# Optimization experiments

Hardware: AMD Instinct MI355X
Metric: run time of the kernel (lower is better)

Reference implementation:

```python
import jax, jax.numpy as jnp
import numpy as np

HEADS = 16
D_MODEL = 1024
D_EXP = 2048  # d_model * expansion_factor
D_HEAD = D_EXP // HEADS
DEPTH = 12
B, L = 2, 2048


def setup_inputs() -> dict:
    key = jax.random.key(0)
    ks = jax.random.split(key, 4)
    x = jax.random.normal(ks[0], (B, L, D_MODEL), dtype=jnp.float32)
    w_in = jax.random.normal(ks[1], (4 * D_EXP, D_MODEL), dtype=jnp.float32) * 0.02
    w_out = jax.random.normal(ks[2], (D_MODEL, D_EXP), dtype=jnp.float32) * (0.02 / np.sqrt(2 * DEPTH))
    # LearnedALiBi init: logspace(0,-6,heads//2,base=2) ++ zeros(heads - heads//2)
    half = HEADS // 2
    slopes = jnp.concatenate([
        jnp.asarray(2.0 ** np.linspace(0.0, -6.0, half), dtype=jnp.float32),
        jnp.zeros((HEADS - half,), dtype=jnp.float32),
    ])
    smear_factor = jnp.linspace(-6.0, 6.0, HEADS, dtype=jnp.float32)
    return {
        "x": x, "w_in": w_in, "w_out": w_out,
        "ln_in_g": jnp.ones((D_MODEL,), jnp.float32), "ln_in_b": jnp.zeros((D_MODEL,), jnp.float32),
        "ln_out_g": jnp.ones((D_MODEL,), jnp.float32), "ln_out_b": jnp.zeros((D_MODEL,), jnp.float32),
        "slopes": slopes, "smear_factor": smear_factor,
    }


def _layernorm(x, g, b, eps=1e-5):
    mu = jnp.mean(x, axis=-1, keepdims=True)
    var = jnp.mean(jnp.square(x - mu), axis=-1, keepdims=True)
    return (x - mu) * jax.lax.rsqrt(var + eps) * g + b


def reference(x, w_in, w_out, ln_in_g, ln_in_b, ln_out_g, ln_out_b, slopes, smear_factor):
    b, l, d = x.shape
    h = _layernorm(x, ln_in_g, ln_in_b)
    qkvp = h @ w_in.T  # (b, l, 4*D_EXP)
    q, k, v, p = jnp.split(qkvp, 4, axis=-1)

    def to_heads(t):  # b i (h d) -> b h i d
        return t.reshape(b, l, HEADS, D_HEAD).transpose(0, 2, 1, 3)

    q, k, v = to_heads(q), to_heads(k), to_heads(v)

    # key smearing: k_i <- (1-s)*k_i + s*k_{i-1}
    smear = jax.nn.sigmoid(smear_factor)[None, :, None, None]
    k_shift = jnp.pad(k, ((0, 0), (0, 0), (1, 0), (0, 0)))[:, :, :-1]
    k = (1.0 - smear) * k + smear * k_shift

    logits = jnp.einsum('bhid,bhjd->bhij', q, k) * (D_HEAD ** -0.5)
    # learned ALiBi bias: j * slope_h  (depends only on key index)
    alibi = jnp.arange(l, dtype=logits.dtype)[None, None, None, :] * slopes[None, :, None, None]
    # causal bias: -1e10 * (1 - tril)
    i_idx = jnp.arange(l)
    causal = jnp.where(i_idx[:, None] >= i_idx[None, :], 0.0, -1e10)[None, None]
    a = jax.nn.softmax(logits + alibi + causal, axis=-1)

    o = jnp.einsum('bhij,bhjd->bhid', a, v)
    o = o.transpose(0, 2, 1, 3).reshape(b, l, D_EXP)  # b h i d -> b i (h d)
    gated = jax.nn.silu(p) * o
    y = gated @ w_out.T
    return _layernorm(y, ln_out_g, ln_out_b)
```

## Files before the change

kernel.cpp:

```cpp
#include <hip/hip_runtime.h>
#include <hip/hip_bf16.h>
#include <stdint.h>


typedef __bf16 bf16;
typedef bf16  bf16x8 __attribute__((ext_vector_type(8)));
typedef bf16  bf16x4 __attribute__((ext_vector_type(4)));
typedef float f32x4  __attribute__((ext_vector_type(4)));

#define SEQ   2048
#define NBATC 2

__device__ __forceinline__ void gld_lds16(const bf16* g, bf16* l) {
  __builtin_amdgcn_global_load_lds((const __attribute__((address_space(1))) void*)g,
                                   (__attribute__((address_space(3))) void*)l, 16, 0, 0);
}

__global__ __launch_bounds__(256) void cvt_kernel(const float* __restrict__ in,
                                                  bf16* __restrict__ out, int n8) {
  int t = blockIdx.x * 256 + threadIdx.x;
  if (t >= n8) return;
  const float4* p = (const float4*)in + (size_t)t * 2;
  float4 a = p[0], b = p[1];
  bf16x8 o;
  o[0] = (bf16)a.x; o[1] = (bf16)a.y; o[2] = (bf16)a.z; o[3] = (bf16)a.w;
  o[4] = (bf16)b.x; o[5] = (bf16)b.y; o[6] = (bf16)b.z; o[7] = (bf16)b.w;
  *((bf16x8*)out + t) = o;
}

template<bool BF16OUT>
__global__ __launch_bounds__(256) void ln_kernel(const float* __restrict__ x,
    const float* __restrict__ gamma, const float* __restrict__ beta,
    void* __restrict__ out) {
  const int row = blockIdx.x;
  const int tid = threadIdx.x;
  float4 v = *(const float4*)(x + (size_t)row * 1024 + tid * 4);
  float s  = v.x + v.y + v.z + v.w;
  float ss = v.x * v.x + v.y * v.y + v.z * v.z + v.w * v.w;
#pragma unroll
  for (int m = 1; m < 64; m <<= 1) { s += __shfl_xor(s, m, 64); ss += __shfl_xor(ss, m, 64); }
  __shared__ float red[8];
  if ((tid & 63) == 0) { red[tid >> 6] = s; red[(tid >> 6) + 4] = ss; }
  __syncthreads();
  s  = red[0] + red[1] + red[2] + red[3];
  ss = red[4] + red[5] + red[6] + red[7];
  const float mu  = s * (1.f / 1024.f);
  const float inv = rsqrtf(ss * (1.f / 1024.f) - mu * mu + 1e-5f);
  float4 g  = *(const float4*)(gamma + tid * 4);
  float4 bb = *(const float4*)(beta  + tid * 4);
  float y0 = (v.x - mu) * inv * g.x + bb.x;
  float y1 = (v.y - mu) * inv * g.y + bb.y;
  float y2 = (v.z - mu) * inv * g.z + bb.z;
  float y3 = (v.w - mu) * inv * g.w + bb.w;
  if (BF16OUT) {
    bf16* o = (bf16*)out + (size_t)row * 1024 + tid * 4;
    o[0] = (bf16)y0; o[1] = (bf16)y1; o[2] = (bf16)y2; o[3] = (bf16)y3;
  } else {
    float* o = (float*)out + (size_t)row * 1024 + tid * 4;
    o[0] = y0; o[1] = y1; o[2] = y2; o[3] = y3;
  }
}

__global__ __launch_bounds__(256) void smear_kernel(const bf16* __restrict__ qkvp,
    const float* __restrict__ smf, bf16* __restrict__ ksm) {
  int t  = blockIdx.x * 256 + threadIdx.x;
  int d8 = t & 15;
  int i  = (t >> 4) & 2047;
  int h  = (t >> 15) & 15;
  int b  = t >> 19;
  float sm = 1.f / (1.f + __expf(-smf[h]));
  const bf16* base = qkvp + (size_t)(b * SEQ + i) * 8192 + 2048 + h * 128 + d8 * 8;
  bf16x8 cur = *(const bf16x8*)base;
  bf16x8 prv = cur;
  if (i > 0) prv = *(const bf16x8*)(base - 8192);
  bf16x8 o;
#pragma unroll
  for (int e = 0; e < 8; e++) {
    float pv = (i > 0) ? (float)prv[e] : 0.f;
    o[e] = (bf16)((1.f - sm) * (float)cur[e] + sm * pv);
  }
  size_t idx = ((size_t)(b * 16 + h) * SEQ + i) * 128 + ((d8 * 8) ^ ((i & 7) << 3));
  *(bf16x8*)(ksm + idx) = o;
}

__global__ __launch_bounds__(256) void vtrans_kernel(const bf16* __restrict__ qkvp,
                                                     bf16* __restrict__ vt) {
  __shared__ bf16 T[128][72];
  const int kt = blockIdx.x, bh = blockIdx.y;
  const int b = bh >> 4, h = bh & 15;
  const int t = threadIdx.x;
  {
    int i = t >> 2, d0 = (t & 3) * 32;
    const bf16* src = qkvp + (size_t)(b * SEQ + kt * 64 + i) * 8192 + 4096 + h * 128 + d0;
#pragma unroll
    for (int m = 0; m < 4; m++) {
      bf16x8 v8 = *(const bf16x8*)(src + m * 8);
#pragma unroll
      for (int e = 0; e < 8; e++) T[d0 + m * 8 + e][i] = v8[e];
    }
  }
  __syncthreads();
  {
    int d = t >> 1, i0 = (t & 1) * 32;
    bf16* dst = vt + (size_t)bh * (SEQ * 128) + (size_t)kt * 8192 + d * 64;
#pragma unroll
    for (int m = 0; m < 4; m++) {
      bf16x8 v8 = *(const bf16x8*)&T[d][i0 + m * 8];
      *(bf16x8*)(dst + (((i0 + m * 8)) ^ ((d & 7) << 3))) = v8;
    }
  }
}

__global__ __launch_bounds__(512) void gemm256(const bf16* __restrict__ A,
    const bf16* __restrict__ Bt, bf16* __restrict__ C, int M, int N, int K,
    int RX, int SX, int SY) {
  __shared__ bf16 As[2][256 * 64];
  __shared__ bf16 Bs[2][256 * 64];
  const int w   = blockIdx.x;
  const int xcd = w & 7, idx = w >> 3;
  const int rx = xcd % RX, ry = xcd / RX;
  const int bx = rx * SX + idx % SX;
  const int by = ry * SY + idx / SX;
  const int tid  = threadIdx.x;
  const int lane = tid & 63, wid = tid >> 6;
  const int l4 = lane >> 4, l16 = lane & 15;
  const int wr = wid >> 2, wc = wid & 3;
  const int rowBase = by * 256, colBase = bx * 256;
  const int NT = K >> 6;

  f32x4 acc[8][4];
  const f32x4 z = {0.f, 0.f, 0.f, 0.f};
#pragma unroll
  for (int i = 0; i < 8; i++)
#pragma unroll
    for (int j = 0; j < 4; j++) acc[i][j] = z;

  auto stage = [&](int kt, int bsel) {
    const int k0 = kt * 64;
    bf16* ad = &As[bsel][tid * 8];
    bf16* bd = &Bs[bsel][tid * 8];
#pragma unroll
    for (int j = 0; j < 4; ++j) {
      const int c   = j * 512 + tid;
      const int row = c >> 3;
      const int sc  = ((c & 7) * 8) ^ ((row & 7) << 3);
      gld_lds16(A  + (size_t)(rowBase + row) * K + k0 + sc, ad + j * 4096);
      gld_lds16(Bt + (size_t)(colBase + row) * K + k0 + sc, bd + j * 4096);
    }
  };

  stage(0, 0);
  for (int t = 0; t < NT; ++t) {
    const int cur = t & 1;
    if (t + 1 < NT) {
      stage(t + 1, cur ^ 1);
      asm volatile("s_waitcnt vmcnt(8)" ::: "memory");
    } else {
      asm volatile("s_waitcnt vmcnt(0)" ::: "memory");
    }
    asm volatile("s_barrier" ::: "memory");
    const bf16* a_ = &As[cur][0];
    const bf16* b_ = &Bs[cur][0];
#pragma unroll
    for (int ks = 0; ks < 2; ++ks) {
      bf16x8 bfr[4];
#pragma unroll
      for (int ni = 0; ni < 4; ++ni) {
        const int br = wc * 64 + ni * 16 + l16;
        bfr[ni] = *(const bf16x8*)&b_[br * 64 + ((ks * 32 + l4 * 8) ^ ((br & 7) << 3))];
      }
#pragma unroll
      for (int mi = 0; mi < 8; ++mi) {
        const int ar = wr * 128 + mi * 16 + l16;
        bf16x8 af = *(const bf16x8*)&a_[ar * 64 + ((ks * 32 + l4 * 8) ^ ((ar & 7) << 3))];
#pragma unroll
        for (int ni = 0; ni < 4; ++ni)
          acc[mi][ni] = __builtin_amdgcn_mfma_f32_16x16x32_bf16(af, bfr[ni], acc[mi][ni], 0, 0, 0);
      }
    }
    asm volatile("s_waitcnt lgkmcnt(0)" ::: "memory");
    asm volatile("s_barrier" ::: "memory");
  }

#pragma unroll
  for (int mi = 0; mi < 8; ++mi)
#pragma unroll
    for (int ni = 0; ni < 4; ++ni) {
      int row = rowBase + wr * 128 + mi * 16 + l4 * 4;
      int col = colBase + wc * 64 + ni * 16 + l16;
#pragma unroll
      for (int r = 0; r < 4; ++r)
        C[(size_t)(row + r) * N + col] = (bf16)acc[mi][ni][r];
    }
}

template<typename OutT>
__global__ __launch_bounds__(256) void gemm_bt(const bf16* __restrict__ A,
    const bf16* __restrict__ Bt, OutT* __restrict__ C, int M, int N, int K,
    int RX, int SX, int SY) {
  __shared__ bf16 As[128 * 32];
  __shared__ bf16 Bs[128 * 32];
  const int w   = blockIdx.x;
  const int xcd = w & 7, idx = w >> 3;
  const int rx = xcd % RX, ry = xcd / RX;
  const int bx = rx * SX + idx % SX;
  const int by = ry * SY + idx / SX;
  const int tid  = threadIdx.x;
  const int lane = tid & 63, wid = tid >> 6;
  const int l4 = lane >> 4, l16 = lane & 15;
  const int wr = wid >> 1, wc = wid & 1;
  const int rowBase = by * 128, colBase = bx * 128;

  const bf16* gA = A  + (size_t)(rowBase + (tid >> 2)) * K + (tid & 3) * 8;
  const bf16* gB = Bt + (size_t)(colBase + (tid >> 2)) * K + (tid & 3) * 8;
  const size_t rowStep = (size_t)64 * K;

  f32x4 acc[4][4];
  const f32x4 z = {0.f, 0.f, 0.f, 0.f};
#pragma unroll
  for (int i = 0; i < 4; i++)
#pragma unroll
    for (int j = 0; j < 4; j++) acc[i][j] = z;

  for (int k0 = 0; k0 < K; k0 += 32) {
    __syncthreads();
    gld_lds16(gA + k0,           &As[tid * 8]);
    gld_lds16(gA + rowStep + k0, &As[2048 + tid * 8]);
    gld_lds16(gB + k0,           &Bs[tid * 8]);
    gld_lds16(gB + rowStep + k0, &Bs[2048 + tid * 8]);
    __syncthreads();
    bf16x8 af[4], bfr[4];
#pragma unroll
    for (int mi = 0; mi < 4; mi++)
      af[mi] = *(const bf16x8*)&As[(wr * 64 + mi * 16 + l16) * 32 + l4 * 8];
#pragma unroll
    for (int ni = 0; ni < 4; ni++)
      bfr[ni] = *(const bf16x8*)&Bs[(wc * 64 + ni * 16 + l16) * 32 + l4 * 8];
#pragma unroll
    for (int mi = 0; mi < 4; mi++)
#pragma unroll
      for (int ni = 0; ni < 4; ni++)
        acc[mi][ni] = __builtin_amdgcn_mfma_f32_16x16x32_bf16(af[mi], bfr[ni], acc[mi][ni], 0, 0, 0);
  }
#pragma unroll
  for (int mi = 0; mi < 4; mi++)
#pragma unroll
    for (int ni = 0; ni < 4; ni++) {
      int row = rowBase + wr * 64 + mi * 16 + l4 * 4;
      int col = colBase + wc * 64 + ni * 16 + l16;
#pragma unroll
      for (int r = 0; r < 4; r++)
        C[(size_t)(row + r) * N + col] = (OutT)acc[mi][ni][r];
    }
}

__global__ __launch_bounds__(256) void attn_kernel(const bf16* __restrict__ qkvp,
    const bf16* __restrict__ ksm, const bf16* __restrict__ vt,
    const float* __restrict__ slopes, bf16* __restrict__ gated) {
  const int w   = blockIdx.x;
  const int l   = (w & 7) * 64 + (w >> 3);
  const int qp  = l & 15;
  const int bh  = l >> 4;
  const int b   = bh >> 4, h = bh & 15;
  const int tid = threadIdx.x, wid = tid >> 6, lane = tid & 63;
  const int l4 = lane >> 4, l16 = lane & 15;
  const int swz = (l16 & 7) << 3;
  const float LOG2E = 1.44269504f;
  const float s2 = 0.08838834764831845f * LOG2E;
  const float slopeL = slopes[h] * LOG2E;

  __shared__ bf16 Kb[2][64 * 128];
  __shared__ bf16 Vb[2][64 * 128];
  __shared__ bf16 P_lds[64 * 64];

  const bf16* ksmB = ksm + (size_t)bh * SEQ * 128;
  const bf16* vtB  = vt  + (size_t)bh * SEQ * 128;

  auto stage = [&](int kt, int bsel) {
    const bf16* ks = ksmB + kt * 8192 + tid * 8;
    const bf16* vs = vtB  + kt * 8192 + tid * 8;
    bf16* kd = &Kb[bsel][tid * 8];
    bf16* vd = &Vb[bsel][tid * 8];
#pragma unroll
    for (int g = 0; g < 4; g++) {
      gld_lds16(ks + g * 2048, kd + g * 2048);
      gld_lds16(vs + g * 2048, vd + g * 2048);
    }
  };

  auto run_strip = [&](int qtile, int ntiles) {
    const int iq = qtile * 64 + wid * 16 + l16;
    bf16x8 qf[4];
    {
      const bf16* qrow = qkvp + (size_t)(b * SEQ + iq) * 8192 + h * 128;
#pragma unroll
      for (int kb = 0; kb < 4; kb++) qf[kb] = *(const bf16x8*)(qrow + kb * 32 + l4 * 8);
    }
    f32x4 oacc[8];
    const f32x4 z = {0.f, 0.f, 0.f, 0.f};
#pragma unroll
    for (int i = 0; i < 8; i++) oacc[i] = z;
    float m2 = -1e38f, lpart = 0.f;

    stage(0, 0);
    for (int t = 0; t < ntiles; ++t) {
      __syncthreads();
      if (t + 1 < ntiles) stage(t + 1, (t + 1) & 1);
      const bf16* K_ = Kb[t & 1];
      const bf16* V_ = Vb[t & 1];
      const int kt = t;

      f32x4 sacc[4];
#pragma unroll
      for (int jf = 0; jf < 4; jf++) {
        bf16x8 kf[4];
#pragma unroll
        for (int kb = 0; kb < 4; kb++)
          kf[kb] = *(const bf16x8*)&K_[(jf * 16 + l16) * 128 + ((kb * 32 + l4 * 8) ^ swz)];
        f32x4 a = z;
#pragma unroll
        for (int kb = 0; kb < 4; kb++)
          a = __builtin_amdgcn_mfma_f32_16x16x32_bf16(kf[kb], qf[kb], a, 0, 0, 0);
        sacc[jf] = a;
      }

      const bool diag = (kt == qtile);
      const int kbase = kt * 64 + l4 * 4;
      float sadj[4][4];
#pragma unroll
      for (int jf = 0; jf < 4; jf++) {
#pragma unroll
        for (int r = 0; r < 4; r++) {
          int j = kbase + jf * 16 + r;
          float v = fmaf(sacc[jf][r], s2, (float)j * slopeL);
          if (diag && j > iq) v = -1e38f;
          sadj[jf][r] = v;
        }
      }

      float mx = sadj[0][0];
#pragma unroll
      for (int jf = 0; jf < 4; jf++)
#pragma unroll
        for (int r = 0; r < 4; r++) mx = fmaxf(mx, sadj[jf][r]);
      mx = fmaxf(mx, __shfl_xor(mx, 16, 64));
      mx = fmaxf(mx, __shfl_xor(mx, 32, 64));

      if (__any(mx > m2 + 14.f)) {
        float mnew  = fmaxf(m2, mx);
        float alpha = __builtin_amdgcn_exp2f(m2 - mnew);
        m2 = mnew;
        lpart *= alpha;
#pragma unroll
        for (int df = 0; df < 8; df++) oacc[df] *= alpha;
      }

      float rs = 0.f;
#pragma unroll
      for (int jf = 0; jf < 4; jf++) {
        bf16x4 pw;
#pragma unroll
        for (int r = 0; r < 4; r++) {
          float pe = __builtin_amdgcn_exp2f(sadj[jf][r] - m2);
          rs += pe;
          pw[r] = (bf16)pe;
        }
        *(bf16x4*)&P_lds[(wid * 16 + l16) * 64 + ((jf * 16 + l4 * 4) ^ swz)] = pw;
      }
      lpart += rs;

#pragma unroll
      for (int kb2 = 0; kb2 < 2; ++kb2) {
        bf16x8 pf = *(const bf16x8*)&P_lds[(wid * 16 + l16) * 64 + ((kb2 * 32 + l4 * 8) ^ swz)];
#pragma unroll
        for (int df = 0; df < 8; df++) {
          bf16x8 vf = *(const bf16x8*)&V_[(df * 16 + l16) * 64 + ((kb2 * 32 + l4 * 8) ^ swz)];
          oacc[df] = __builtin_amdgcn_mfma_f32_16x16x32_bf16(vf, pf, oacc[df], 0, 0, 0);
        }
      }
    }

    lpart += __shfl_xor(lpart, 16, 64);
    lpart += __shfl_xor(lpart, 32, 64);
    const float linv = 1.f / lpart;
    const bf16* pgrow = qkvp + (size_t)(b * SEQ + iq) * 8192 + 6144 + h * 128;
    bf16* grow = gated + (size_t)(b * SEQ + iq) * 2048 + h * 128;
#pragma unroll
    for (int df = 0; df < 8; df++) {
      const int d0 = df * 16 + l4 * 4;
      bf16x4 pg4 = *(const bf16x4*)(pgrow + d0);
      bf16x4 o4;
#pragma unroll
      for (int r = 0; r < 4; r++) {
        float o  = oacc[df][r] * linv;
        float pg = (float)pg4[r];
        float silu = pg / (1.f + __expf(-pg));
        o4[r] = (bf16)(silu * o);
      }
      *(bf16x4*)(grow + d0) = o4;
    }
  };

  run_strip(qp, qp + 1);
  __syncthreads();
  run_strip(31 - qp, 32 - qp);
}

extern "C" void kernel_launch(void* const* d_in, const int* in_sizes, int n_in,
                              void* d_out, int out_size, void* d_ws, size_t ws_size,
                              hipStream_t stream) {
  (void)in_sizes; (void)n_in; (void)out_size; (void)ws_size;
  const float* x      = (const float*)d_in[0];
  const float* w_in   = (const float*)d_in[1];
  const float* w_out  = (const float*)d_in[2];
  const float* lnig   = (const float*)d_in[3];
  const float* lnib   = (const float*)d_in[4];
  const float* lnog   = (const float*)d_in[5];
  const float* lnob   = (const float*)d_in[6];
  const float* slopes = (const float*)d_in[7];
  const float* smf    = (const float*)d_in[8];
  float* out = (float*)d_out;

  char* ws = (char*)d_ws;
  size_t off = 0;
  bf16* hb      = (bf16*)(ws + off); off += (size_t)4096 * 1024 * 2;
  bf16* w_in_b  = (bf16*)(ws + off); off += (size_t)8192 * 1024 * 2;
  bf16* w_out_b = (bf16*)(ws + off); off += (size_t)1024 * 2048 * 2;
  bf16* qkvp    = (bf16*)(ws + off); off += (size_t)4096 * 8192 * 2;
  bf16* ksm     = (bf16*)(ws + off); off += (size_t)32 * 2048 * 128 * 2;
  bf16* gated   = (bf16*)(ws + off); off += (size_t)4096 * 2048 * 2;
  float* yb     = (float*)(ws + off); off += (size_t)4096 * 1024 * 4;
  bf16* vt      = (bf16*)yb;

  cvt_kernel<<<4096, 256, 0, stream>>>(w_in,  w_in_b,  8388608 / 8);
  cvt_kernel<<<1024, 256, 0, stream>>>(w_out, w_out_b, 2097152 / 8);
  ln_kernel<true><<<4096, 256, 0, stream>>>(x, lnig, lnib, hb);
  gemm256<<<512, 512, 0, stream>>>(hb, w_in_b, qkvp, 4096, 8192, 1024, 4, 8, 8);
  smear_kernel<<<4096, 256, 0, stream>>>(qkvp, smf, ksm);
  vtrans_kernel<<<dim3(32, 32), 256, 0, stream>>>(qkvp, vt);
  attn_kernel<<<512, 256, 0, stream>>>(qkvp, ksm, vt, slopes, gated);
  gemm_bt<float><<<256, 256, 0, stream>>>(gated, w_out_b, yb, 4096, 1024, 2048, 1, 8, 4);
  ln_kernel<false><<<4096, 256, 0, stream>>>(yb, lnog, lnob, out);
}
```

Measured before the change: 241.4 us.

## Fuse smear and V-transpose kernels; restructure attention into 128-row 8-wave blocks

Merges the key-smearing and V-transpose kernels into one prep kernel, which removes a launch and runs both over the same tile grid. The attention kernel switches from 256-thread blocks that each process two paired 64-row strips to 512-thread blocks that each own one 128-row query tile. Blocks are ordered heaviest-first with an XCD-aware head mapping. K/V loads are staged with explicit vmcnt waits and raw barriers so the next tile's global-to-LDS load overlaps compute. In exchange the causal work is no longer balanced per block, because each block now has a different tile count, and the manual waitcnt/barrier scheme is fragile.

```diff
diff --git a/kernel.cpp b/kernel.cpp
--- a/kernel.cpp
+++ b/kernel.cpp
@@ -61,34 +61,13 @@
   }
 }
 
-__global__ __launch_bounds__(256) void smear_kernel(const bf16* __restrict__ qkvp,
-    const float* __restrict__ smf, bf16* __restrict__ ksm) {
-  int t  = blockIdx.x * 256 + threadIdx.x;
-  int d8 = t & 15;
-  int i  = (t >> 4) & 2047;
-  int h  = (t >> 15) & 15;
-  int b  = t >> 19;
-  float sm = 1.f / (1.f + __expf(-smf[h]));
-  const bf16* base = qkvp + (size_t)(b * SEQ + i) * 8192 + 2048 + h * 128 + d8 * 8;
-  bf16x8 cur = *(const bf16x8*)base;
-  bf16x8 prv = cur;
-  if (i > 0) prv = *(const bf16x8*)(base - 8192);
-  bf16x8 o;
-#pragma unroll
-  for (int e = 0; e < 8; e++) {
-    float pv = (i > 0) ? (float)prv[e] : 0.f;
-    o[e] = (bf16)((1.f - sm) * (float)cur[e] + sm * pv);
-  }
-  size_t idx = ((size_t)(b * 16 + h) * SEQ + i) * 128 + ((d8 * 8) ^ ((i & 7) << 3));
-  *(bf16x8*)(ksm + idx) = o;
-}
-
-__global__ __launch_bounds__(256) void vtrans_kernel(const bf16* __restrict__ qkvp,
-                                                     bf16* __restrict__ vt) {
+__global__ __launch_bounds__(256) void prep_kernel(const bf16* __restrict__ qkvp,
+    const float* __restrict__ smf, bf16* __restrict__ ksm, bf16* __restrict__ vt) {
   __shared__ bf16 T[128][72];
   const int kt = blockIdx.x, bh = blockIdx.y;
   const int b = bh >> 4, h = bh & 15;
   const int t = threadIdx.x;
+
   {
     int i = t >> 2, d0 = (t & 3) * 32;
     const bf16* src = qkvp + (size_t)(b * SEQ + kt * 64 + i) * 8192 + 4096 + h * 128 + d0;
@@ -99,6 +78,29 @@
       for (int e = 0; e < 8; e++) T[d0 + m * 8 + e][i] = v8[e];
     }
   }
+
+  {
+    float sm = 1.f / (1.f + __expf(-smf[h]));
+#pragma unroll
+    for (int j = 0; j < 4; j++) {
+      int c  = j * 256 + t;
+      int il = c >> 4, d8 = c & 15;
+      int i  = kt * 64 + il;
+      const bf16* base = qkvp + (size_t)(b * SEQ + i) * 8192 + 2048 + h * 128 + d8 * 8;
+      bf16x8 cur = *(const bf16x8*)base;
+      bf16x8 prv = cur;
+      if (i > 0) prv = *(const bf16x8*)(base - 8192);
+      bf16x8 o;
+#pragma unroll
+      for (int e = 0; e < 8; e++) {
+        float pv = (i > 0) ? (float)prv[e] : 0.f;
+        o[e] = (bf16)((1.f - sm) * (float)cur[e] + sm * pv);
+      }
+      size_t idx = ((size_t)bh * SEQ + i) * 128 + ((d8 * 8) ^ ((i & 7) << 3));
+      *(bf16x8*)(ksm + idx) = o;
+    }
+  }
+
   __syncthreads();
   {
     int d = t >> 1, i0 = (t & 1) * 32;
@@ -254,13 +256,13 @@
     }
 }
 
-__global__ __launch_bounds__(256) void attn_kernel(const bf16* __restrict__ qkvp,
+__global__ __launch_bounds__(512, 4) void attn_kernel(const bf16* __restrict__ qkvp,
     const bf16* __restrict__ ksm, const bf16* __restrict__ vt,
     const float* __restrict__ slopes, bf16* __restrict__ gated) {
-  const int w   = blockIdx.x;
-  const int l   = (w & 7) * 64 + (w >> 3);
-  const int qp  = l & 15;
-  const int bh  = l >> 4;
+  const int w     = blockIdx.x;
+  const int xcd   = w & 7, r0 = w >> 3;
+  const int bh    = xcd * 4 + (r0 & 3);
+  const int qtile = 15 - (r0 >> 2);
   const int b   = bh >> 4, h = bh & 15;
   const int tid = threadIdx.x, wid = tid >> 6, lane = tid & 63;
   const int l4 = lane >> 4, l16 = lane & 15;
@@ -271,139 +273,137 @@
 
   __shared__ bf16 Kb[2][64 * 128];
   __shared__ bf16 Vb[2][64 * 128];
-  __shared__ bf16 P_lds[64 * 64];
+  __shared__ bf16 P_lds[128 * 64];
 
   const bf16* ksmB = ksm + (size_t)bh * SEQ * 128;
   const bf16* vtB  = vt  + (size_t)bh * SEQ * 128;
 
   auto stage = [&](int kt, int bsel) {
-    const bf16* ks = ksmB + kt * 8192 + tid * 8;
-    const bf16* vs = vtB  + kt * 8192 + tid * 8;
-    bf16* kd = &Kb[bsel][tid * 8];
-    bf16* vd = &Vb[bsel][tid * 8];
-#pragma unroll
-    for (int g = 0; g < 4; g++) {
-      gld_lds16(ks + g * 2048, kd + g * 2048);
-      gld_lds16(vs + g * 2048, vd + g * 2048);
+#pragma unroll
+    for (int j = 0; j < 2; j++) {
+      const int c = j * 512 + tid;
+      gld_lds16(ksmB + (size_t)kt * 8192 + c * 8, &Kb[bsel][c * 8]);
+      gld_lds16(vtB  + (size_t)kt * 8192 + c * 8, &Vb[bsel][c * 8]);
     }
   };
 
-  auto run_strip = [&](int qtile, int ntiles) {
-    const int iq = qtile * 64 + wid * 16 + l16;
-    bf16x8 qf[4];
-    {
-      const bf16* qrow = qkvp + (size_t)(b * SEQ + iq) * 8192 + h * 128;
-#pragma unroll
-      for (int kb = 0; kb < 4; kb++) qf[kb] = *(const bf16x8*)(qrow + kb * 32 + l4 * 8);
-    }
-    f32x4 oacc[8];
-    const f32x4 z = {0.f, 0.f, 0.f, 0.f};
-#pragma unroll
-    for (int i = 0; i < 8; i++) oacc[i] = z;
-    float m2 = -1e38f, lpart = 0.f;
-
-    stage(0, 0);
-    for (int t = 0; t < ntiles; ++t) {
-      __syncthreads();
-      if (t + 1 < ntiles) stage(t + 1, (t + 1) & 1);
-      const bf16* K_ = Kb[t & 1];
-      const bf16* V_ = Vb[t & 1];
-      const int kt = t;
-
-      f32x4 sacc[4];
-#pragma unroll
-      for (int jf = 0; jf < 4; jf++) {
-        bf16x8 kf[4];
-#pragma unroll
-        for (int kb = 0; kb < 4; kb++)
-          kf[kb] = *(const bf16x8*)&K_[(jf * 16 + l16) * 128 + ((kb * 32 + l4 * 8) ^ swz)];
-        f32x4 a = z;
-#pragma unroll
-        for (int kb = 0; kb < 4; kb++)
-          a = __builtin_amdgcn_mfma_f32_16x16x32_bf16(kf[kb], qf[kb], a, 0, 0, 0);
-        sacc[jf] = a;
-      }
-
-      const bool diag = (kt == qtile);
-      const int kbase = kt * 64 + l4 * 4;
-      float sadj[4][4];
-#pragma unroll
-      for (int jf = 0; jf < 4; jf++) {
-#pragma unroll
-        for (int r = 0; r < 4; r++) {
-          int j = kbase + jf * 16 + r;
-          float v = fmaf(sacc[jf][r], s2, (float)j * slopeL);
-          if (diag && j > iq) v = -1e38f;
-          sadj[jf][r] = v;
-        }
-      }
-
-      float mx = sadj[0][0];
-#pragma unroll
-      for (int jf = 0; jf < 4; jf++)
-#pragma unroll
-        for (int r = 0; r < 4; r++) mx = fmaxf(mx, sadj[jf][r]);
-      mx = fmaxf(mx, __shfl_xor(mx, 16, 64));
-      mx = fmaxf(mx, __shfl_xor(mx, 32, 64));
-
-      if (__any(mx > m2 + 14.f)) {
-        float mnew  = fmaxf(m2, mx);
-        float alpha = __builtin_amdgcn_exp2f(m2 - mnew);
-        m2 = mnew;
-        lpart *= alpha;
-#pragma unroll
-        for (int df = 0; df < 8; df++) oacc[df] *= alpha;
-      }
-
-      float rs = 0.f;
-#pragma unroll
-      for (int jf = 0; jf < 4; jf++) {
-        bf16x4 pw;
-#pragma unroll
-        for (int r = 0; r < 4; r++) {
-          float pe = __builtin_amdgcn_exp2f(sadj[jf][r] - m2);
-          rs += pe;
-          pw[r] = (bf16)pe;
-        }
-        *(bf16x4*)&P_lds[(wid * 16 + l16) * 64 + ((jf * 16 + l4 * 4) ^ swz)] = pw;
-      }
-      lpart += rs;
-
-#pragma unroll
-      for (int kb2 = 0; kb2 < 2; ++kb2) {
-        bf16x8 pf = *(const bf16x8*)&P_lds[(wid * 16 + l16) * 64 + ((kb2 * 32 + l4 * 8) ^ swz)];
-#pragma unroll
-        for (int df = 0; df < 8; df++) {
-          bf16x8 vf = *(const bf16x8*)&V_[(df * 16 + l16) * 64 + ((kb2 * 32 + l4 * 8) ^ swz)];
-          oacc[df] = __builtin_amdgcn_mfma_f32_16x16x32_bf16(vf, pf, oacc[df], 0, 0, 0);
-        }
-      }
-    }
-
-    lpart += __shfl_xor(lpart, 16, 64);
-    lpart += __shfl_xor(lpart, 32, 64);
-    const float linv = 1.f / lpart;
-    const bf16* pgrow = qkvp + (size_t)(b * SEQ + iq) * 8192 + 6144 + h * 128;
-    bf16* grow = gated + (size_t)(b * SEQ + iq) * 2048 + h * 128;
-#pragma unroll
-    for (int df = 0; df < 8; df++) {
-      const int d0 = df * 16 + l4 * 4;
-      bf16x4 pg4 = *(const bf16x4*)(pgrow + d0);
-      bf16x4 o4;
+  const int iq = qtile * 128 + wid * 16 + l16;
+  bf16x8 qf[4];
+  {
+    const bf16* qrow = qkvp + (size_t)(b * SEQ + iq) * 8192 + h * 128;
+#pragma unroll
+    for (int kb = 0; kb < 4; kb++) qf[kb] = *(const bf16x8*)(qrow + kb * 32 + l4 * 8);
+  }
+  f32x4 oacc[8];
+  const f32x4 z = {0.f, 0.f, 0.f, 0.f};
+#pragma unroll
+  for (int i = 0; i < 8; i++) oacc[i] = z;
+  float m2 = -1e38f, lpart = 0.f;
+
+  const int nt = 2 * qtile + 2;
+  stage(0, 0);
+  for (int t = 0; t < nt; ++t) {
+    const int cur = t & 1;
+    if (t + 1 < nt) {
+      stage(t + 1, cur ^ 1);
+      asm volatile("s_waitcnt vmcnt(4)" ::: "memory");
+    } else {
+      asm volatile("s_waitcnt vmcnt(0)" ::: "memory");
+    }
+    __builtin_amdgcn_sched_barrier(0);
+    __builtin_amdgcn_s_barrier();
+    const bf16* K_ = Kb[cur];
+    const bf16* V_ = Vb[cur];
+
+    f32x4 sacc[4];
+#pragma unroll
+    for (int jf = 0; jf < 4; jf++) {
+      f32x4 a = z;
+#pragma unroll
+      for (int kb = 0; kb < 4; kb++) {
+        bf16x8 kf = *(const bf16x8*)&K_[(jf * 16 + l16) * 128 + ((kb * 32 + l4 * 8) ^ swz)];
+        a = __builtin_amdgcn_mfma_f32_16x16x32_bf16(kf, qf[kb], a, 0, 0, 0);
+      }
+      sacc[jf] = a;
+    }
+
+    const bool diag = (t >= 2 * qtile);
+    const int kbase = t * 64 + l4 * 4;
+#pragma unroll
+    for (int jf = 0; jf < 4; jf++) {
 #pragma unroll
       for (int r = 0; r < 4; r++) {
-        float o  = oacc[df][r] * linv;
-        float pg = (float)pg4[r];
-        float silu = pg / (1.f + __expf(-pg));
-        o4[r] = (bf16)(silu * o);
-      }
-      *(bf16x4*)(grow + d0) = o4;
-    }
-  };
-
-  run_strip(qp, qp + 1);
-  __syncthreads();
-  run_strip(31 - qp, 32 - qp);
+        int j = kbase + jf * 16 + r;
+        float v = fmaf(sacc[jf][r], s2, (float)j * slopeL);
+        if (diag && j > iq) v = -1e38f;
+        sacc[jf][r] = v;
+      }
+    }
+
+    float mx = sacc[0][0];
+#pragma unroll
+    for (int jf = 0; jf < 4; jf++)
+#pragma unroll
+      for (int r = 0; r < 4; r++) mx = fmaxf(mx, sacc[jf][r]);
+    mx = fmaxf(mx, __shfl_xor(mx, 16, 64));
+    mx = fmaxf(mx, __shfl_xor(mx, 32, 64));
+
+    if (__any(mx > m2 + 14.f)) {
+      float mnew  = fmaxf(m2, mx);
+      float alpha = __builtin_amdgcn_exp2f(m2 - mnew);
+      m2 = mnew;
+      lpart *= alpha;
+#pragma unroll
+      for (int df = 0; df < 8; df++) oacc[df] *= alpha;
+    }
+
+    float rs = 0.f;
+#pragma unroll
+    for (int jf = 0; jf < 4; jf++) {
+      bf16x4 pw;
+#pragma unroll
+      for (int r = 0; r < 4; r++) {
+        float pe = __builtin_amdgcn_exp2f(sacc[jf][r] - m2);
+        rs += pe;
+        pw[r] = (bf16)pe;
+      }
+      *(bf16x4*)&P_lds[(wid * 16 + l16) * 64 + ((jf * 16 + l4 * 4) ^ swz)] = pw;
+    }
+    lpart += rs;
+
+#pragma unroll
+    for (int kb2 = 0; kb2 < 2; ++kb2) {
+      bf16x8 pf = *(const bf16x8*)&P_lds[(wid * 16 + l16) * 64 + ((kb2 * 32 + l4 * 8) ^ swz)];
+#pragma unroll
+      for (int df = 0; df < 8; df++) {
+        bf16x8 vf = *(const bf16x8*)&V_[(df * 16 + l16) * 64 + ((kb2 * 32 + l4 * 8) ^ swz)];
+        oacc[df] = __builtin_amdgcn_mfma_f32_16x16x32_bf16(vf, pf, oacc[df], 0, 0, 0);
+      }
+    }
+
+    asm volatile("s_waitcnt lgkmcnt(0)" ::: "memory");
+    __builtin_amdgcn_s_barrier();
+  }
+
+  lpart += __shfl_xor(lpart, 16, 64);
+  lpart += __shfl_xor(lpart, 32, 64);
+  const float linv = 1.f / lpart;
+  const bf16* pgrow = qkvp + (size_t)(b * SEQ + iq) * 8192 + 6144 + h * 128;
+  bf16* grow = gated + (size_t)(b * SEQ + iq) * 2048 + h * 128;
+#pragma unroll
+  for (int df = 0; df < 8; df++) {
+    const int d0 = df * 16 + l4 * 4;
+    bf16x4 pg4 = *(const bf16x4*)(pgrow + d0);
+    bf16x4 o4;
+#pragma unroll
+    for (int r = 0; r < 4; r++) {
+      float o  = oacc[df][r] * linv;
+      float pg = (float)pg4[r];
+      float silu = pg / (1.f + __expf(-pg));
+      o4[r] = (bf16)(silu * o);
+    }
+    *(bf16x4*)(grow + d0) = o4;
+  }
 }
 
 extern "C" void kernel_launch(void* const* d_in, const int* in_sizes, int n_in,
@@ -436,9 +436,8 @@
   cvt_kernel<<<1024, 256, 0, stream>>>(w_out, w_out_b, 2097152 / 8);
   ln_kernel<true><<<4096, 256, 0, stream>>>(x, lnig, lnib, hb);
   gemm256<<<512, 512, 0, stream>>>(hb, w_in_b, qkvp, 4096, 8192, 1024, 4, 8, 8);
-  smear_kernel<<<4096, 256, 0, stream>>>(qkvp, smf, ksm);
-  vtrans_kernel<<<dim3(32, 32), 256, 0, stream>>>(qkvp, vt);
-  attn_kernel<<<512, 256, 0, stream>>>(qkvp, ksm, vt, slopes, gated);
+  prep_kernel<<<dim3(32, 32), 256, 0, stream>>>(qkvp, smf, ksm, vt);
+  attn_kernel<<<512, 512, 0, stream>>>(qkvp, ksm, vt, slopes, gated);
   gemm_bt<float><<<256, 256, 0, stream>>>(gated, w_out_b, yb, 4096, 1024, 2048, 1, 8, 4);
   ln_kernel<false><<<4096, 256, 0, stream>>>(yb, lnog, lnob, out);
 }
```

New measurement: 236.1 us. 2.2% less time.
